# Performance work log

Measured on AMD Instinct MI355X. Metric: run time of the kernel, lower is better.

## Reference

```python
import jax, jax.numpy as jnp
import numpy as np

NEG_SLOPE = 0.2


def _gat_layer(h, adj, W, a, n_heads, head_dim, is_concat):
    # h: [n, f_in]; adj: [n, n, 1] int; W: [f_in, n_heads*head_dim]; a: [2*head_dim]
    n = h.shape[0]
    g = (h @ W).reshape(n, n_heads, head_dim)                # [n, H, d]
    a_src, a_dst = a[:head_dim], a[head_dim:]
    s_src = jnp.einsum('nhd,d->nh', g, a_src)                # contribution of g_i
    s_dst = jnp.einsum('nhd,d->nh', g, a_dst)                # contribution of g_j
    # e[i, j, h] = leaky_relu(a_l . g_i + a_r . g_j)  (exact decomposition of attn Linear)
    e = jax.nn.leaky_relu(s_src[:, None, :] + s_dst[None, :, :], NEG_SLOPE)  # [n, n, H]
    e = jnp.where(adj > 0, e, -jnp.inf)                      # adj [n,n,1] broadcasts over heads
    attn = jax.nn.softmax(e, axis=1)                         # softmax over neighbors j
    out = jnp.einsum('ijh,jhd->ihd', attn, g)                # aggregate neighbor features
    if is_concat:
        return out.reshape(n, n_heads * head_dim)
    return out.mean(axis=1)


def setup_inputs() -> dict:
    key = jax.random.key(0)
    ks = jax.random.split(key, 8)
    B, N, F_IN, H, HD1 = 4096, 46, 1024, 8, 32
    x = jax.random.normal(ks[0], (B, N, F_IN), dtype=jnp.float32)
    adj_mat = jnp.ones((N, N, 1), dtype=jnp.int32)
    W1 = jax.random.normal(ks[1], (F_IN, H * HD1), dtype=jnp.float32) * 0.03
    a1 = jax.random.normal(ks[2], (2 * HD1,), dtype=jnp.float32) * 0.1
    W2 = jax.random.normal(ks[3], (H * HD1, 64), dtype=jnp.float32) * 0.06
    a2 = jax.random.normal(ks[4], (2 * 64,), dtype=jnp.float32) * 0.1
    Wm1 = jax.random.normal(ks[5], (N, 12), dtype=jnp.float32) * 0.15
    bm1 = jnp.zeros((12,), dtype=jnp.float32)
    Wm2 = jax.random.normal(ks[6], (12, 1), dtype=jnp.float32) * 0.3
    bm2 = jnp.zeros((1,), dtype=jnp.float32)
    return {"x": x, "adj_mat": adj_mat, "W1": W1, "a1": a1, "W2": W2, "a2": a2,
            "Wm1": Wm1, "bm1": bm1, "Wm2": Wm2, "bm2": bm2}


def reference(x, adj_mat, W1, a1, W2, a2, Wm1, bm1, Wm2, bm2):
    # Dropout is identity (eval mode / p used as 0.0).
    def per_sample(h):                                        # h: [46, 1024]
        h1 = jax.nn.elu(_gat_layer(h, adj_mat, W1, a1, 8, 32, True))   # [46, 256]
        h2 = _gat_layer(h1, adj_mat, W2, a2, 1, 64, False)              # [46, 64]
        pooled = h2.mean(axis=1)                                        # [46]
        z = pooled @ Wm1 + bm1                                          # [12]
        z = z @ Wm2 + bm2                                               # [1]
        return jax.nn.sigmoid(z)                                        # [1]
    return jax.vmap(per_sample)(x)                            # [B, 1]
```

## Files before the change

### kernel.cpp

```cpp
#include <hip/hip_runtime.h>

#define NN  46
#define FIN 1024
#define C1  256
#define C2  64

typedef __attribute__((ext_vector_type(4))) float f32x4;
typedef __attribute__((ext_vector_type(8))) short bf16x8;

#define A_OFF   0
#define B_OFF   47840
#define G1_OFF  0
#define SS_OFF  30720
#define SD_OFF  32192
#define H1_OFF  47840
#define G2_OFF  0
#define S2S_OFF 12704
#define S2D_OFF 12896
#define GM_OFF  13088
#define PL_OFF  13280
#define Z1_OFF  13472
#define SMEM_SZ 80608

__device__ __forceinline__ float bf2f(unsigned short u) {
  union { unsigned int i; float f; } v; v.i = ((unsigned int)u) << 16; return v.f;
}
__device__ __forceinline__ unsigned short f2bf(float f) {
  unsigned int u = __float_as_uint(f);
  u += 0x7fffu + ((u >> 16) & 1u);
  return (unsigned short)(u >> 16);
}
__device__ __forceinline__ float lrelu(float x) { return x > 0.f ? x : 0.2f * x; }

__device__ __forceinline__ void glds16(const void* g, void* l) {
  __builtin_amdgcn_global_load_lds(
      (const __attribute__((address_space(1))) unsigned int*)g,
      (__attribute__((address_space(3))) unsigned int*)l, 16, 0, 0);
}

__global__ __launch_bounds__(512, 4) void gat_main(
    const float* __restrict__ x,
    const float* __restrict__ a1, const float* __restrict__ a2,
    const float* __restrict__ Wm1, const float* __restrict__ bm1,
    const float* __restrict__ Wm2, const float* __restrict__ bm2,
    const unsigned short* __restrict__ W1T, const unsigned short* __restrict__ W2T,
    float* __restrict__ out)
{
  __shared__ __attribute__((aligned(128))) unsigned char smem[SMEM_SZ];
  unsigned short* const Asm = (unsigned short*)(smem + A_OFF);
  unsigned short* const G1  = (unsigned short*)(smem + G1_OFF);
  unsigned short* const H1  = (unsigned short*)(smem + H1_OFF);
  float* const SS  = (float*)(smem + SS_OFF);
  float* const SD  = (float*)(smem + SD_OFF);
  float* const G2  = (float*)(smem + G2_OFF);
  float* const S2S = (float*)(smem + S2S_OFF);
  float* const S2D = (float*)(smem + S2D_OFF);
  float* const GM  = (float*)(smem + GM_OFF);
  float* const PL  = (float*)(smem + PL_OFF);
  float* const Z1  = (float*)(smem + Z1_OFF);

  const int tid  = threadIdx.x;
  const int wave = tid >> 6;
  const int lane = tid & 63;
  const int l16  = lane & 15;
  const int q4   = lane >> 4;
  const int kq8  = q4 * 8;
  const int rq4  = q4 * 4;
  const float* __restrict__ xb = x + (size_t)blockIdx.x * (NN * FIN);

  float4 xv[12];
#pragma unroll
  for (int i = 0; i < 12; ++i) {
    int idx = tid + i * 512;
    if (idx < 5888) { int r = idx >> 7, c = idx & 127;
      xv[i] = *(const float4*)(xb + r * FIN + c * 4); }
  }
#pragma unroll
  for (int i = 0; i < 12; ++i) {
    int idx = tid + i * 512;
    if (idx < 5888) { int r = idx >> 7, c = idx & 127;
      ushort4 u; u.x = f2bf(xv[i].x); u.y = f2bf(xv[i].y); u.z = f2bf(xv[i].z); u.w = f2bf(xv[i].w);
      *(ushort4*)(Asm + r * 520 + c * 4) = u; }
  }
#pragma unroll
  for (int i = 0; i < 12; ++i) {
    int idx = tid + i * 512;
    if (idx < 5888) { int r = idx >> 7, c = idx & 127;
      xv[i] = *(const float4*)(xb + r * FIN + 512 + c * 4); }
  }

  f32x4 acc[3][2];
#pragma unroll
  for (int i = 0; i < 3; ++i) { acc[i][0] = 0; acc[i][1] = 0; }

  for (int kt = 0; kt < 16; ++kt) {
    if (kt == 8) {
#pragma unroll
      for (int i = 0; i < 12; ++i) {
        int idx = tid + i * 512;
        if (idx < 5888) { int r = idx >> 7, c = idx & 127;
          ushort4 u; u.x = f2bf(xv[i].x); u.y = f2bf(xv[i].y); u.z = f2bf(xv[i].z); u.w = f2bf(xv[i].w);
          *(ushort4*)(Asm + r * 520 + c * 4) = u; }
      }
    }
#pragma unroll
    for (int i = 0; i < 4; ++i) {
      int rr = wave * 32 + i * 8 + (lane >> 3);
      int j  = lane & 7;
      const unsigned short* src = W1T + (size_t)rr * FIN + kt * 64 + (((j ^ (rr & 7)) << 3));
      glds16(src, smem + B_OFF + (wave * 32 + i * 8) * 128);
    }
    __syncthreads();

    const int ktl = kt & 7;
#pragma unroll
    for (int ks = 0; ks < 2; ++ks) {
      bf16x8 af[3], bfr[2];
#pragma unroll
      for (int rt = 0; rt < 3; ++rt)
        af[rt] = *(const bf16x8*)(Asm + (rt * 16 + l16) * 520 + ktl * 64 + ks * 32 + kq8);
#pragma unroll
      for (int ct = 0; ct < 2; ++ct) {
        int brow  = wave * 32 + ct * 16 + l16;
        int chunk = (ks * 4 + q4) ^ (l16 & 7);
        bfr[ct] = *(const bf16x8*)(smem + B_OFF + brow * 128 + chunk * 16);
      }
#pragma unroll
      for (int rt = 0; rt < 3; ++rt)
#pragma unroll
        for (int ct = 0; ct < 2; ++ct)
          acc[rt][ct] = __builtin_amdgcn_mfma_f32_16x16x32_bf16(af[rt], bfr[ct], acc[rt][ct], 0, 0, 0);
    }
    __syncthreads();
  }

#pragma unroll
  for (int rt = 0; rt < 3; ++rt)
#pragma unroll
    for (int ct = 0; ct < 2; ++ct)
#pragma unroll
      for (int r = 0; r < 4; ++r) {
        int row = rt * 16 + rq4 + r;
        int d   = ct * 16 + l16;
        if (row < NN) G1[row * 320 + wave * 40 + d] = f2bf(acc[rt][ct][r]);
      }
  __syncthreads();

  if (tid < NN * 8) {
    int n = tid >> 3, h = tid & 7;
    const unsigned short* g = G1 + n * 320 + h * 40;
    float ss = 0.f, sd = 0.f;
#pragma unroll 8
    for (int d = 0; d < 32; ++d) {
      float gv = bf2f(g[d]);
      ss += gv * a1[d];
      sd += gv * a1[32 + d];
    }
    SS[tid] = ss; SD[tid] = sd;
  }
  H1[46 * 264 + (tid >> 8) * 264 + (tid & 255)] = 0;
  __syncthreads();

  if (tid < NN * 8) {
    int i = tid >> 3, h = tid & 7;
    float ssi = SS[tid];
    float m = -1e30f;
    for (int j = 0; j < NN; ++j) m = fmaxf(m, lrelu(ssi + SD[j * 8 + h]));
    float av[32];
#pragma unroll
    for (int d = 0; d < 32; ++d) av[d] = 0.f;
    float sum = 0.f;
    for (int j = 0; j < NN; ++j) {
      float p = __expf(lrelu(ssi + SD[j * 8 + h]) - m);
      sum += p;
      const unsigned short* g = G1 + j * 320 + h * 40;
#pragma unroll
      for (int d4 = 0; d4 < 8; ++d4) {
        ushort4 v = *(const ushort4*)(g + d4 * 4);
        av[d4 * 4 + 0] += p * bf2f(v.x);
        av[d4 * 4 + 1] += p * bf2f(v.y);
        av[d4 * 4 + 2] += p * bf2f(v.z);
        av[d4 * 4 + 3] += p * bf2f(v.w);
      }
    }
    float inv = 1.f / sum;
#pragma unroll
    for (int d2 = 0; d2 < 16; ++d2) {
      float o0 = av[2 * d2] * inv;
      float o1 = av[2 * d2 + 1] * inv;
      o0 = o0 > 0.f ? o0 : __expf(o0) - 1.f;
      o1 = o1 > 0.f ? o1 : __expf(o1) - 1.f;
      ushort2 st; st.x = f2bf(o0); st.y = f2bf(o1);
      *(ushort2*)(H1 + i * 264 + h * 32 + d2 * 2) = st;
    }
  }
  __syncthreads();

  for (int tile = wave; tile < 12; tile += 8) {
    int rt = tile >> 2, ct = tile & 3;
    f32x4 ac = 0;
#pragma unroll
    for (int ks = 0; ks < 8; ++ks) {
      bf16x8 af = *(const bf16x8*)(H1 + (rt * 16 + l16) * 264 + ks * 32 + kq8);
      bf16x8 bw = *(const bf16x8*)(W2T + (ct * 16 + l16) * 256 + ks * 32 + kq8);
      ac = __builtin_amdgcn_mfma_f32_16x16x32_bf16(af, bw, ac, 0, 0, 0);
    }
#pragma unroll
    for (int r = 0; r < 4; ++r) {
      int row = rt * 16 + rq4 + r;
      if (row < NN) G2[row * 69 + ct * 16 + l16] = ac[r];
    }
  }
  __syncthreads();

  if (tid < NN) {
    const float* g = G2 + tid * 69;
    float ss = 0.f, sd = 0.f, gm = 0.f;
#pragma unroll 8
    for (int d = 0; d < 64; ++d) {
      float gv = g[d];
      ss += gv * a2[d]; sd += gv * a2[64 + d]; gm += gv;
    }
    S2S[tid] = ss; S2D[tid] = sd; GM[tid] = gm * (1.f / 64.f);
  }
  __syncthreads();

  if (tid < NN) {
    float si = S2S[tid];
    float m = -1e30f;
    for (int j = 0; j < NN; ++j) m = fmaxf(m, lrelu(si + S2D[j]));
    float sum = 0.f, accp = 0.f;
    for (int j = 0; j < NN; ++j) {
      float p = __expf(lrelu(si + S2D[j]) - m);
      sum += p; accp += p * GM[j];
    }
    PL[tid] = accp / sum;
  }
  __syncthreads();

  if (tid < 12) {
    float z = 0.f;
    for (int i = 0; i < NN; ++i) z += PL[i] * Wm1[i * 12 + tid];
    Z1[tid] = z + bm1[tid];
  }
  __syncthreads();
  if (tid == 0) {
    float z = 0.f;
#pragma unroll
    for (int mm = 0; mm < 12; ++mm) z += Z1[mm] * Wm2[mm];
    z += bm2[0];
    out[blockIdx.x] = 1.f / (1.f + __expf(-z));
  }
}

__global__ void gat_prep(const float* __restrict__ W1, const float* __restrict__ W2,
                         unsigned short* __restrict__ W1T, unsigned short* __restrict__ W2T)
{
  int id = blockIdx.x * 256 + threadIdx.x;
  if (id < FIN * C1) {
    int k = id >> 8, n = id & 255;
    W1T[n * FIN + k] = f2bf(W1[id]);
  }
  if (id < C1 * C2) {
    int k = id >> 6, n = id & 63;
    W2T[n * C1 + k] = f2bf(W2[id]);
  }
}

extern "C" void kernel_launch(void* const* d_in, const int* in_sizes, int n_in,
                              void* d_out, int out_size, void* d_ws, size_t ws_size,
                              hipStream_t stream)
{
  const float* x   = (const float*)d_in[0];
  const float* W1  = (const float*)d_in[2];
  const float* a1  = (const float*)d_in[3];
  const float* W2  = (const float*)d_in[4];
  const float* a2  = (const float*)d_in[5];
  const float* Wm1 = (const float*)d_in[6];
  const float* bm1 = (const float*)d_in[7];
  const float* Wm2 = (const float*)d_in[8];
  const float* bm2 = (const float*)d_in[9];
  float* out = (float*)d_out;

  unsigned short* W1T = (unsigned short*)d_ws;
  unsigned short* W2T = (unsigned short*)((char*)d_ws + (size_t)FIN * C1 * 2);

  int B = in_sizes[0] / (NN * FIN);

  hipLaunchKernelGGL(gat_prep, dim3(1024), dim3(256), 0, stream, W1, W2, W1T, W2T);
  hipLaunchKernelGGL(gat_main, dim3(B), dim3(512), 0, stream,
                     x, a1, a2, Wm1, bm1, Wm2, bm2, W1T, W2T, out);
}
```

Measured before the change: 391.2 us.

## Compute layer-1 attention aggregation with MFMA and stream x in quarter chunks

Layer-1 neighbour aggregation now builds the bf16 softmax probability matrix P per head and multiplies it by a transposed G1 tile with 32x32x16 MFMA, replacing the scalar per-thread loop over neighbours. The attention scores are computed directly from the GEMM accumulators with lane shuffles, so the separate pass over G1 goes away. The x tile is double-buffered in quarter-width chunks instead of halves, which lowers register pressure for the prefetch. In exchange there are more shared-memory layout regions and extra barriers, and the probabilities are rounded to bf16.

```diff
diff --git a/kernel.cpp b/kernel.cpp
--- a/kernel.cpp
+++ b/kernel.cpp
@@ -6,21 +6,25 @@
 #define C2  64
 
 typedef __attribute__((ext_vector_type(4))) float f32x4;
+typedef __attribute__((ext_vector_type(16))) float f32x16;
 typedef __attribute__((ext_vector_type(8))) short bf16x8;
 
-#define A_OFF   0
-#define B_OFF   47840
-#define G1_OFF  0
-#define SS_OFF  30720
-#define SD_OFF  32192
-#define H1_OFF  47840
-#define G2_OFF  0
-#define S2S_OFF 12704
-#define S2D_OFF 12896
-#define GM_OFF  13088
-#define PL_OFF  13280
-#define Z1_OFF  13472
-#define SMEM_SZ 80608
+#define AB0_OFF 0
+#define AB1_OFF 24288
+#define B_OFF   48576
+#define G1T_OFF 0
+#define P_OFF   28672
+#define SS_OFF  69888
+#define SD_OFF  71424
+#define SI_OFF  72960
+#define H1_OFF  0
+#define G2_OFF  25600
+#define S2S_OFF 38400
+#define S2D_OFF 38656
+#define GM_OFF  38912
+#define PL_OFF  39168
+#define Z1_OFF  39424
+#define SMEM_SZ 81344
 
 __device__ __forceinline__ float bf2f(unsigned short u) {
   union { unsigned int i; float f; } v; v.i = ((unsigned int)u) << 16; return v.f;
@@ -37,6 +41,19 @@
       (const __attribute__((address_space(1))) unsigned int*)g,
       (__attribute__((address_space(3))) unsigned int*)l, 16, 0, 0);
 }
+
+#define XLOAD(q) do { _Pragma("unroll") \
+  for (int i_ = 0; i_ < 6; ++i_) { int idx_ = tid + i_ * 512; \
+    if (idx_ < 2944) { int r_ = idx_ >> 6, c_ = idx_ & 63; \
+      xv[i_] = *(const float4*)(xb + r_ * FIN + (q) * 256 + c_ * 4); } } } while (0)
+
+#define XWRITE(b) do { unsigned short* Ap_ = (unsigned short*)(smem + ((b) ? AB1_OFF : AB0_OFF)); \
+  _Pragma("unroll") \
+  for (int i_ = 0; i_ < 6; ++i_) { int idx_ = tid + i_ * 512; \
+    if (idx_ < 2944) { int r_ = idx_ >> 6, c_ = idx_ & 63; \
+      ushort4 u_; u_.x = f2bf(xv[i_].x); u_.y = f2bf(xv[i_].y); \
+      u_.z = f2bf(xv[i_].z); u_.w = f2bf(xv[i_].w); \
+      *(ushort4*)(Ap_ + r_ * 264 + c_ * 4) = u_; } } } while (0)
 
 __global__ __launch_bounds__(512, 4) void gat_main(
     const float* __restrict__ x,
@@ -47,17 +64,6 @@
     float* __restrict__ out)
 {
   __shared__ __attribute__((aligned(128))) unsigned char smem[SMEM_SZ];
-  unsigned short* const Asm = (unsigned short*)(smem + A_OFF);
-  unsigned short* const G1  = (unsigned short*)(smem + G1_OFF);
-  unsigned short* const H1  = (unsigned short*)(smem + H1_OFF);
-  float* const SS  = (float*)(smem + SS_OFF);
-  float* const SD  = (float*)(smem + SD_OFF);
-  float* const G2  = (float*)(smem + G2_OFF);
-  float* const S2S = (float*)(smem + S2S_OFF);
-  float* const S2D = (float*)(smem + S2D_OFF);
-  float* const GM  = (float*)(smem + GM_OFF);
-  float* const PL  = (float*)(smem + PL_OFF);
-  float* const Z1  = (float*)(smem + Z1_OFF);
 
   const int tid  = threadIdx.x;
   const int wave = tid >> 6;
@@ -66,59 +72,42 @@
   const int q4   = lane >> 4;
   const int kq8  = q4 * 8;
   const int rq4  = q4 * 4;
+  const int l32  = lane & 31;
+  const int hh   = lane >> 5;
   const float* __restrict__ xb = x + (size_t)blockIdx.x * (NN * FIN);
 
-  float4 xv[12];
-#pragma unroll
-  for (int i = 0; i < 12; ++i) {
-    int idx = tid + i * 512;
-    if (idx < 5888) { int r = idx >> 7, c = idx & 127;
-      xv[i] = *(const float4*)(xb + r * FIN + c * 4); }
-  }
-#pragma unroll
-  for (int i = 0; i < 12; ++i) {
-    int idx = tid + i * 512;
-    if (idx < 5888) { int r = idx >> 7, c = idx & 127;
-      ushort4 u; u.x = f2bf(xv[i].x); u.y = f2bf(xv[i].y); u.z = f2bf(xv[i].z); u.w = f2bf(xv[i].w);
-      *(ushort4*)(Asm + r * 520 + c * 4) = u; }
-  }
-#pragma unroll
-  for (int i = 0; i < 12; ++i) {
-    int idx = tid + i * 512;
-    if (idx < 5888) { int r = idx >> 7, c = idx & 127;
-      xv[i] = *(const float4*)(xb + r * FIN + 512 + c * 4); }
-  }
+  float4 xv[6];
+
+  XLOAD(0); XWRITE(0); XLOAD(1);
 
   f32x4 acc[3][2];
 #pragma unroll
   for (int i = 0; i < 3; ++i) { acc[i][0] = 0; acc[i][1] = 0; }
 
   for (int kt = 0; kt < 16; ++kt) {
-    if (kt == 8) {
-#pragma unroll
-      for (int i = 0; i < 12; ++i) {
-        int idx = tid + i * 512;
-        if (idx < 5888) { int r = idx >> 7, c = idx & 127;
-          ushort4 u; u.x = f2bf(xv[i].x); u.y = f2bf(xv[i].y); u.z = f2bf(xv[i].z); u.w = f2bf(xv[i].w);
-          *(ushort4*)(Asm + r * 520 + c * 4) = u; }
-      }
-    }
 #pragma unroll
     for (int i = 0; i < 4; ++i) {
       int rr = wave * 32 + i * 8 + (lane >> 3);
       int j  = lane & 7;
-      const unsigned short* src = W1T + (size_t)rr * FIN + kt * 64 + (((j ^ (rr & 7)) << 3));
+      const unsigned short* src = W1T + (size_t)rr * FIN + kt * 64 + ((j ^ (rr & 7)) << 3);
       glds16(src, smem + B_OFF + (wave * 32 + i * 8) * 128);
     }
     __syncthreads();
 
-    const int ktl = kt & 7;
+    if ((kt & 3) == 0 && kt < 12) {
+      int qw = (kt >> 2) + 1;
+      XWRITE(qw & 1);
+      if (qw < 3) XLOAD(qw + 1);
+    }
+
+    const unsigned short* Ap = (const unsigned short*)(smem + (((kt >> 2) & 1) ? AB1_OFF : AB0_OFF));
+    const int ktl = kt & 3;
 #pragma unroll
     for (int ks = 0; ks < 2; ++ks) {
       bf16x8 af[3], bfr[2];
 #pragma unroll
       for (int rt = 0; rt < 3; ++rt)
-        af[rt] = *(const bf16x8*)(Asm + (rt * 16 + l16) * 520 + ktl * 64 + ks * 32 + kq8);
+        af[rt] = *(const bf16x8*)(Ap + (rt * 16 + l16) * 264 + ktl * 64 + ks * 32 + kq8);
 #pragma unroll
       for (int ct = 0; ct < 2; ++ct) {
         int brow  = wave * 32 + ct * 16 + l16;
@@ -135,121 +124,174 @@
   }
 
 #pragma unroll
-  for (int rt = 0; rt < 3; ++rt)
-#pragma unroll
-    for (int ct = 0; ct < 2; ++ct)
+  for (int i = 0; i < 4; ++i) {
+    int idx = tid + i * 512;
+    if (idx < 1792) { f32x4 z = 0; *(f32x4*)(smem + idx * 16) = z; }
+  }
+  __syncthreads();
+
+  {
+    unsigned short* g1T = (unsigned short*)(smem + G1T_OFF);
+    float* SSp = (float*)(smem + SS_OFF);
+    float* SDp = (float*)(smem + SD_OFF);
+    float a1s[2], a1d[2];
+#pragma unroll
+    for (int ct = 0; ct < 2; ++ct) {
+      a1s[ct] = a1[ct * 16 + l16];
+      a1d[ct] = a1[32 + ct * 16 + l16];
+    }
+#pragma unroll
+    for (int rt = 0; rt < 3; ++rt)
 #pragma unroll
       for (int r = 0; r < 4; ++r) {
         int row = rt * 16 + rq4 + r;
-        int d   = ct * 16 + l16;
-        if (row < NN) G1[row * 320 + wave * 40 + d] = f2bf(acc[rt][ct][r]);
-      }
-  __syncthreads();
-
-  if (tid < NN * 8) {
-    int n = tid >> 3, h = tid & 7;
-    const unsigned short* g = G1 + n * 320 + h * 40;
-    float ss = 0.f, sd = 0.f;
+        float ss = acc[rt][0][r] * a1s[0] + acc[rt][1][r] * a1s[1];
+        float sd = acc[rt][0][r] * a1d[0] + acc[rt][1][r] * a1d[1];
+#pragma unroll
+        for (int m = 1; m < 16; m <<= 1) {
+          ss += __shfl_xor(ss, m);
+          sd += __shfl_xor(sd, m);
+        }
+        if (row < NN) {
+#pragma unroll
+          for (int ct = 0; ct < 2; ++ct)
+            g1T[wave * 1792 + (ct * 16 + l16) * 56 + row] = f2bf(acc[rt][ct][r]);
+          if (l16 == 0) { SSp[wave * 48 + row] = ss; SDp[wave * 48 + row] = sd; }
+        }
+      }
+  }
+  __syncthreads();
+
+  if (lane < NN) {
+    const float* SSp = (const float*)(smem + SS_OFF);
+    const float* SDp = (const float*)(smem + SD_OFF);
+    float ssi = SSp[wave * 48 + lane];
+    float m = -1e30f;
+    for (int j = 0; j < NN; ++j) m = fmaxf(m, lrelu(ssi + SDp[wave * 48 + j]));
+    float sum = 0.f;
+    unsigned short* Pr = (unsigned short*)(smem + P_OFF) + wave * 2576 + lane * 56;
+    for (int jb = 0; jb < 48; jb += 4) {
+      ushort4 u;
+#pragma unroll
+      for (int jj = 0; jj < 4; ++jj) {
+        int j = jb + jj;
+        float e = 0.f;
+        if (j < NN) { e = __expf(lrelu(ssi + SDp[wave * 48 + j]) - m); sum += e; }
+        ((unsigned short*)&u)[jj] = f2bf(e);
+      }
+      *(ushort4*)(Pr + jb) = u;
+    }
+    ((float*)(smem + SI_OFF))[wave * 48 + lane] = 1.f / sum;
+  }
+  __syncthreads();
+
+  f32x16 pv0 = 0, pv1 = 0;
+  {
+    const unsigned short* Pb = (const unsigned short*)(smem + P_OFF);
+    const unsigned short* Gt = (const unsigned short*)(smem + G1T_OFF);
+#pragma unroll
+    for (int ks = 0; ks < 3; ++ks) {
+      bf16x8 bfrag = *(const bf16x8*)(Gt + wave * 1792 + l32 * 56 + ks * 16 + hh * 8);
+      bf16x8 a0 = *(const bf16x8*)(Pb + wave * 2576 + l32 * 56 + ks * 16 + hh * 8);
+      bf16x8 a1f = *(const bf16x8*)(Pb + wave * 2576 + (32 + l32) * 56 + ks * 16 + hh * 8);
+      pv0 = __builtin_amdgcn_mfma_f32_32x32x16_bf16(a0, bfrag, pv0, 0, 0, 0);
+      pv1 = __builtin_amdgcn_mfma_f32_32x32x16_bf16(a1f, bfrag, pv1, 0, 0, 0);
+    }
+  }
+  __syncthreads();
+
+  {
+    unsigned short* H1p = (unsigned short*)(smem + H1_OFF);
+    const float* SIp = (const float*)(smem + SI_OFF);
+#pragma unroll
+    for (int mt = 0; mt < 2; ++mt)
+#pragma unroll
+      for (int rg = 0; rg < 16; ++rg) {
+        int row = mt * 32 + (rg & 3) + 8 * (rg >> 2) + 4 * hh;
+        if (row < NN) {
+          float v = (mt ? pv1[rg] : pv0[rg]) * SIp[wave * 48 + row];
+          v = v > 0.f ? v : __expf(v) - 1.f;
+          H1p[row * 264 + wave * 32 + l32] = f2bf(v);
+        }
+      }
+    if (tid < 132) *(unsigned long long*)((char*)H1p + 46 * 528 + tid * 8) = 0ull;
+  }
+  __syncthreads();
+
+  {
+    const unsigned short* H1p = (const unsigned short*)(smem + H1_OFF);
+    float* G2p = (float*)(smem + G2_OFF);
+    for (int tile = wave; tile < 12; tile += 8) {
+      int rt = tile >> 2, ct = tile & 3;
+      f32x4 a4 = 0;
+#pragma unroll
+      for (int ks = 0; ks < 8; ++ks) {
+        bf16x8 af = *(const bf16x8*)(H1p + (rt * 16 + l16) * 264 + ks * 32 + kq8);
+        bf16x8 bw = *(const bf16x8*)(W2T + (ct * 16 + l16) * 256 + ks * 32 + kq8);
+        a4 = __builtin_amdgcn_mfma_f32_16x16x32_bf16(af, bw, a4, 0, 0, 0);
+      }
+#pragma unroll
+      for (int r = 0; r < 4; ++r) {
+        int row = rt * 16 + rq4 + r;
+        if (row < NN) G2p[row * 69 + ct * 16 + l16] = a4[r];
+      }
+    }
+  }
+  __syncthreads();
+
+  {
+    const float* G2p = (const float*)(smem + G2_OFF);
+    float* S2S = (float*)(smem + S2S_OFF);
+    float* S2D = (float*)(smem + S2D_OFF);
+    float* GM  = (float*)(smem + GM_OFF);
+    if (tid < NN) {
+      const float* g = G2p + tid * 69;
+      float ss = 0.f, sd = 0.f, gm = 0.f;
 #pragma unroll 8
-    for (int d = 0; d < 32; ++d) {
-      float gv = bf2f(g[d]);
-      ss += gv * a1[d];
-      sd += gv * a1[32 + d];
-    }
-    SS[tid] = ss; SD[tid] = sd;
-  }
-  H1[46 * 264 + (tid >> 8) * 264 + (tid & 255)] = 0;
-  __syncthreads();
-
-  if (tid < NN * 8) {
-    int i = tid >> 3, h = tid & 7;
-    float ssi = SS[tid];
-    float m = -1e30f;
-    for (int j = 0; j < NN; ++j) m = fmaxf(m, lrelu(ssi + SD[j * 8 + h]));
-    float av[32];
-#pragma unroll
-    for (int d = 0; d < 32; ++d) av[d] = 0.f;
-    float sum = 0.f;
-    for (int j = 0; j < NN; ++j) {
-      float p = __expf(lrelu(ssi + SD[j * 8 + h]) - m);
-      sum += p;
-      const unsigned short* g = G1 + j * 320 + h * 40;
-#pragma unroll
-      for (int d4 = 0; d4 < 8; ++d4) {
-        ushort4 v = *(const ushort4*)(g + d4 * 4);
-        av[d4 * 4 + 0] += p * bf2f(v.x);
-        av[d4 * 4 + 1] += p * bf2f(v.y);
-        av[d4 * 4 + 2] += p * bf2f(v.z);
-        av[d4 * 4 + 3] += p * bf2f(v.w);
-      }
-    }
-    float inv = 1.f / sum;
-#pragma unroll
-    for (int d2 = 0; d2 < 16; ++d2) {
-      float o0 = av[2 * d2] * inv;
-      float o1 = av[2 * d2 + 1] * inv;
-      o0 = o0 > 0.f ? o0 : __expf(o0) - 1.f;
-      o1 = o1 > 0.f ? o1 : __expf(o1) - 1.f;
-      ushort2 st; st.x = f2bf(o0); st.y = f2bf(o1);
-      *(ushort2*)(H1 + i * 264 + h * 32 + d2 * 2) = st;
-    }
-  }
-  __syncthreads();
-
-  for (int tile = wave; tile < 12; tile += 8) {
-    int rt = tile >> 2, ct = tile & 3;
-    f32x4 ac = 0;
-#pragma unroll
-    for (int ks = 0; ks < 8; ++ks) {
-      bf16x8 af = *(const bf16x8*)(H1 + (rt * 16 + l16) * 264 + ks * 32 + kq8);
-      bf16x8 bw = *(const bf16x8*)(W2T + (ct * 16 + l16) * 256 + ks * 32 + kq8);
-      ac = __builtin_amdgcn_mfma_f32_16x16x32_bf16(af, bw, ac, 0, 0, 0);
-    }
-#pragma unroll
-    for (int r = 0; r < 4; ++r) {
-      int row = rt * 16 + rq4 + r;
-      if (row < NN) G2[row * 69 + ct * 16 + l16] = ac[r];
-    }
-  }
-  __syncthreads();
-
-  if (tid < NN) {
-    const float* g = G2 + tid * 69;
-    float ss = 0.f, sd = 0.f, gm = 0.f;
-#pragma unroll 8
-    for (int d = 0; d < 64; ++d) {
-      float gv = g[d];
-      ss += gv * a2[d]; sd += gv * a2[64 + d]; gm += gv;
-    }
-    S2S[tid] = ss; S2D[tid] = sd; GM[tid] = gm * (1.f / 64.f);
-  }
-  __syncthreads();
-
-  if (tid < NN) {
-    float si = S2S[tid];
-    float m = -1e30f;
-    for (int j = 0; j < NN; ++j) m = fmaxf(m, lrelu(si + S2D[j]));
-    float sum = 0.f, accp = 0.f;
-    for (int j = 0; j < NN; ++j) {
-      float p = __expf(lrelu(si + S2D[j]) - m);
-      sum += p; accp += p * GM[j];
-    }
-    PL[tid] = accp / sum;
-  }
-  __syncthreads();
-
-  if (tid < 12) {
-    float z = 0.f;
-    for (int i = 0; i < NN; ++i) z += PL[i] * Wm1[i * 12 + tid];
-    Z1[tid] = z + bm1[tid];
-  }
-  __syncthreads();
-  if (tid == 0) {
-    float z = 0.f;
-#pragma unroll
-    for (int mm = 0; mm < 12; ++mm) z += Z1[mm] * Wm2[mm];
-    z += bm2[0];
-    out[blockIdx.x] = 1.f / (1.f + __expf(-z));
+      for (int d = 0; d < 64; ++d) {
+        float gv = g[d];
+        ss += gv * a2[d]; sd += gv * a2[64 + d]; gm += gv;
+      }
+      S2S[tid] = ss; S2D[tid] = sd; GM[tid] = gm * (1.f / 64.f);
+    }
+  }
+  __syncthreads();
+
+  {
+    const float* S2S = (const float*)(smem + S2S_OFF);
+    const float* S2D = (const float*)(smem + S2D_OFF);
+    const float* GM  = (const float*)(smem + GM_OFF);
+    float* PL = (float*)(smem + PL_OFF);
+    if (tid < NN) {
+      float si = S2S[tid];
+      float m = -1e30f;
+      for (int j = 0; j < NN; ++j) m = fmaxf(m, lrelu(si + S2D[j]));
+      float sum = 0.f, accp = 0.f;
+      for (int j = 0; j < NN; ++j) {
+        float p = __expf(lrelu(si + S2D[j]) - m);
+        sum += p; accp += p * GM[j];
+      }
+      PL[tid] = accp / sum;
+    }
+  }
+  __syncthreads();
+
+  {
+    const float* PL = (const float*)(smem + PL_OFF);
+    float* Z1 = (float*)(smem + Z1_OFF);
+    if (tid < 12) {
+      float z = 0.f;
+      for (int i = 0; i < NN; ++i) z += PL[i] * Wm1[i * 12 + tid];
+      Z1[tid] = z + bm1[tid];
+    }
+    __syncthreads();
+    if (tid == 0) {
+      float z = 0.f;
+#pragma unroll
+      for (int mm = 0; mm < 12; ++mm) z += Z1[mm] * Wm2[mm];
+      z += bm2[0];
+      out[blockIdx.x] = 1.f / (1.f + __expf(-z));
+    }
   }
 }
 
```

Result: faster. 329.1 us (-15.9%).
